# Performance work log

Hardware: AMD Instinct MI355X
Metric: run time of the kernel (lower is better)

## Reference

```python
import jax, jax.numpy as jnp
import numpy as np

B, S, HID, NH = 4, 2048, 128, 8
D_MODEL = HID * NH  # per-Q/K/V dim = 1024


def setup_inputs() -> dict:
    key = jax.random.key(0)
    k1, k2, k3, k4, k5 = jax.random.split(key, 5)
    return {
        "x": jax.random.normal(k1, (B, S, HID), dtype=jnp.float32),
        "W_qkv": jax.random.normal(k2, (HID, 3 * D_MODEL), dtype=jnp.float32) * 0.02,
        "b_qkv": jax.random.normal(k3, (3 * D_MODEL,), dtype=jnp.float32) * 0.02,
        "W_o": jax.random.normal(k4, (D_MODEL, HID), dtype=jnp.float32) * 0.02,
        "b_o": jax.random.normal(k5, (HID,), dtype=jnp.float32) * 0.02,
        "num_heads": NH,
    }


def reference(x, W_qkv, b_qkv, W_o, b_o, num_heads):
    b, s, _ = x.shape
    qkv = x @ W_qkv + b_qkv                      # [b, s, 3*d_model]
    Q, K, V = jnp.split(qkv, 3, axis=2)          # each [b, s, d_model]
    d_full = Q.shape[-1]                         # n_heads*headsize (faithful to source)
    hs = d_full // num_heads
    # [b, s, h*hs] -> [b, h, s, hs]
    def to_heads(t):
        return t.reshape(b, s, num_heads, hs).transpose(0, 2, 1, 3)
    Qh, Kh, Vh = to_heads(Q), to_heads(K), to_heads(V)
    scores = jnp.einsum('bhsc,bhtc->bhst', Qh, Kh)
    # multiplicative upper-triangular mask (faithful quirk of source)
    tri = jnp.triu(jnp.ones((s, s), dtype=scores.dtype))
    A_pre = scores * tri / jnp.sqrt(jnp.asarray(d_full, dtype=scores.dtype))
    # softmax over dim=1 == heads axis (faithful quirk of source)
    A = jax.nn.softmax(A_pre, axis=1)
    out = jnp.einsum('bhst,bhtc->bhsc', A, Vh)   # [b, h, s, hs]
    out = out.transpose(0, 2, 1, 3).reshape(b, s, d_full)
    return out @ W_o + b_o                        # [b, s, hidden]
```

## Files before the change

kernel.cpp:

```cpp
#include <hip/hip_runtime.h>
#include <hip/hip_bf16.h>

#define SEQ 2048
#define NHEAD 8
#define HDIM 128

typedef __attribute__((ext_vector_type(8))) short bf16x8;
typedef __attribute__((ext_vector_type(4))) float f32x4;
typedef long i64;
typedef unsigned long long u64;

static __device__ __forceinline__ short f2b(float f) {
  union { float f; unsigned u; } v; v.f = f;
  unsigned r = (v.u + 0x7FFFu + ((v.u >> 16) & 1u)) >> 16;
  return (short)(unsigned short)r;
}
static __device__ __forceinline__ float b2f(short b) {
  union { unsigned u; float f; } v; v.u = ((unsigned)(unsigned short)b) << 16;
  return v.f;
}
static __device__ __forceinline__ unsigned f2e4m3(float x) {
  union { float f; unsigned u; } v; v.f = x;
  unsigned s = (v.u >> 24) & 0x80u;
  unsigned a = v.u & 0x7FFFFFFFu;
  if (a > 0x43E00000u) a = 0x43E00000u;
  if (a < 0x3C800000u) {
    union { unsigned u; float f; } w; w.u = a;
    return s | (unsigned)(int)(w.f * 512.0f + 0.5f);
  }
  a += 0x7FFFFu + ((a >> 20) & 1u);
  return s | (((a >> 23) - 120u) << 3) | ((a >> 20) & 7u);
}

#if defined(__has_builtin)
#if __has_builtin(__builtin_amdgcn_cvt_pk_fp8_f32)
#define HAVE_HW_FP8 1
#endif
#endif
static __device__ __forceinline__ unsigned cvt_pk_fp8(float a, float b) {
#ifdef HAVE_HW_FP8
  return (unsigned)__builtin_amdgcn_cvt_pk_fp8_f32(a, b, 0, false) & 0xFFFFu;
#else
  return f2e4m3(a) | (f2e4m3(b) << 8);
#endif
}
static __device__ __forceinline__ unsigned cvt_fp8_1(float a) {
  return cvt_pk_fp8(a, 0.0f) & 0xFFu;
}

#define BARRIER_RAW() asm volatile("s_waitcnt lgkmcnt(0)\n\ts_barrier" ::: "memory")

__global__ __launch_bounds__(256) void k_cvt_x(const float* __restrict__ x,
                                               short* __restrict__ xb) {
  int i = blockIdx.x * blockDim.x + threadIdx.x;
  const float4* p = reinterpret_cast<const float4*>(x) + (size_t)i * 2;
  float4 a = p[0], c = p[1];
  bf16x8 o;
  o[0] = f2b(a.x); o[1] = f2b(a.y); o[2] = f2b(a.z); o[3] = f2b(a.w);
  o[4] = f2b(c.x); o[5] = f2b(c.y); o[6] = f2b(c.z); o[7] = f2b(c.w);
  reinterpret_cast<bf16x8*>(xb)[i] = o;
}

__global__ __launch_bounds__(256) void k_wqkv(const float* __restrict__ w,
                                              short* __restrict__ wt) {
  int tid = blockIdx.x * blockDim.x + threadIdx.x;
  int k = tid & 127, j = tid >> 7;
  wt[tid] = f2b(w[(size_t)k * 3072 + j]);
}

__global__ __launch_bounds__(256) void k_wo(const float* __restrict__ w,
                                            short* __restrict__ wt) {
  int tid = blockIdx.x * blockDim.x + threadIdx.x;
  int k = tid & 1023, c = tid >> 10;
  wt[tid] = f2b(w[(size_t)k * 128 + c]);
}

__global__ __launch_bounds__(256) void k_qkv(const short* __restrict__ xb,
                                             const short* __restrict__ wqt,
                                             const float* __restrict__ bias,
                                             unsigned char* __restrict__ Qf,
                                             unsigned char* __restrict__ Kf,
                                             unsigned char* __restrict__ Vt) {
  int wave = threadIdx.x >> 6, lane = threadIdx.x & 63;
  int lr = lane & 15, lg = lane >> 4;
  int m0 = blockIdx.y * 64 + wave * 16;
  int j0 = blockIdx.x * 128;

  bf16x8 a[4];
#pragma unroll
  for (int ks = 0; ks < 4; ++ks)
    a[ks] = *reinterpret_cast<const bf16x8*>(xb + (size_t)(m0 + lr) * 128 + ks * 32 + lg * 8);

  f32x4 acc[8];
#pragma unroll
  for (int nf = 0; nf < 8; ++nf) acc[nf] = (f32x4){0.f, 0.f, 0.f, 0.f};

#pragma unroll
  for (int ks = 0; ks < 4; ++ks) {
#pragma unroll
    for (int nf = 0; nf < 8; ++nf) {
      bf16x8 bfr = *reinterpret_cast<const bf16x8*>(
          wqt + (size_t)(j0 + nf * 16 + lr) * 128 + ks * 32 + lg * 8);
      acc[nf] = __builtin_amdgcn_mfma_f32_16x16x32_bf16(a[ks], bfr, acc[nf], 0, 0, 0);
    }
  }

  int bb = m0 >> 11;
  int sbase = m0 & 2047;
#pragma unroll
  for (int nf = 0; nf < 8; ++nf) {
    int j = j0 + nf * 16 + lr;
    float bv = bias[j];
    int sel = j >> 10;
    int jj = j & 1023;
    int h = jj >> 7, c = jj & 127;
    size_t bh = (size_t)(bb * NHEAD + h);
    if (sel == 2) {
      unsigned lo = cvt_pk_fp8((acc[nf][0] + bv) * 16.0f, (acc[nf][1] + bv) * 16.0f);
      unsigned hi = cvt_pk_fp8((acc[nf][2] + bv) * 16.0f, (acc[nf][3] + bv) * 16.0f);
      *reinterpret_cast<unsigned*>(Vt + (bh * HDIM + c) * SEQ + sbase + lg * 4) =
          lo | (hi << 16);
    } else {
      unsigned char* dst = (sel ? Kf : Qf);
#pragma unroll
      for (int r = 0; r < 4; ++r) {
        int s = sbase + lg * 4 + r;
        dst[(bh * SEQ + s) * HDIM + c] = (unsigned char)cvt_fp8_1((acc[nf][r] + bv) * 4.0f);
      }
    }
  }
}

__global__ __launch_bounds__(256) void k_tot(const unsigned char* __restrict__ Vt,
                                             float* __restrict__ Tot8) {
  __shared__ float lut[256];
  {
    int t = threadIdx.x;
    unsigned e = (t >> 3) & 15u, m = t & 7u;
    float mag = e ? ldexpf((float)(8 + m), (int)e - 10) : ldexpf((float)m, -9);
    lut[t] = (t & 128) ? -mag : mag;
  }
  __syncthreads();
  int wave = threadIdx.x >> 6, lane = threadIdx.x & 63;
  int row = blockIdx.x * 4 + wave;
  const unsigned char* p = Vt + (size_t)row * SEQ;
  float s = 0.f;
#pragma unroll
  for (int k = 0; k < 4; ++k) {
    u64 v = *reinterpret_cast<const u64*>(p + k * 512 + lane * 8);
#pragma unroll
    for (int j = 0; j < 8; ++j) s += lut[(unsigned)(v >> (8 * j)) & 255u];
  }
#pragma unroll
  for (int off = 32; off > 0; off >>= 1) s += __shfl_down(s, off, 64);
  if (lane == 0) Tot8[row] = s * 0.0078125f;
}

__global__ __launch_bounds__(512, 4) void k_attn(const unsigned char* __restrict__ Qf,
                                                 const unsigned char* __restrict__ Kf,
                                                 const unsigned char* __restrict__ Vt,
                                                 short* __restrict__ Part) {
  __shared__ float Sm[8][32][36];
  __shared__ unsigned char Pm[8][32][40];

  int tid = threadIdx.x;
  int h = (__builtin_amdgcn_readfirstlane(tid) >> 6) & 7;
  int lane = tid & 63, lr = lane & 15, lg = lane >> 4;
  int bid = blockIdx.x;
  int xcd = bid & 7, slot = bid >> 3;
  int b = xcd >> 1, tc = xcd & 1;
  int c0 = (slot < 32) ? slot : (95 - slot);
  int rb = c0 * 32;

  const unsigned char* Qh = Qf + ((size_t)(b * NHEAD + h)) * SEQ * HDIM;
  const unsigned char* Kh = Kf + ((size_t)(b * NHEAD + h)) * SEQ * HDIM;
  const unsigned char* Vh = Vt + ((size_t)(b * NHEAD + h)) * HDIM * SEQ;
  short* PartT = Part + (size_t)tc * (size_t)(4 * SEQ) * 1024;

  int sl = tid >> 4;
  int t2 = (tid & 15) * 2;
  const float SC = 0.001953125f;

  i64 qa[2][4];
#pragma unroll
  for (int rf = 0; rf < 2; ++rf)
#pragma unroll
    for (int ks = 0; ks < 4; ++ks)
      qa[rf][ks] = *reinterpret_cast<const i64*>(
          Qh + (size_t)(rb + rf * 16 + lr) * HDIM + ks * 32 + lg * 8);

  f32x4 oa[2][8];
#pragma unroll
  for (int rf = 0; rf < 2; ++rf)
#pragma unroll
    for (int cf = 0; cf < 8; ++cf) oa[rf][cf] = (f32x4){0.f, 0.f, 0.f, 0.f};

  int ttF = 62 + tc;

#pragma unroll 1
  for (int tt = ttF; tt >= c0; tt -= 2) {
    int t0 = tt * 32;
    i64 vf[8];
#pragma unroll
    for (int cf = 0; cf < 8; ++cf)
      vf[cf] = *reinterpret_cast<const i64*>(Vh + (size_t)(cf * 16 + lr) * SEQ + t0 + lg * 8);
    i64 kf[2][4];
#pragma unroll
    for (int nf = 0; nf < 2; ++nf)
#pragma unroll
      for (int ks = 0; ks < 4; ++ks)
        kf[nf][ks] = *reinterpret_cast<const i64*>(
            Kh + (size_t)(t0 + nf * 16 + lr) * HDIM + ks * 32 + lg * 8);

    __builtin_amdgcn_s_setprio(1);
#pragma unroll
    for (int rf = 0; rf < 2; ++rf) {
      f32x4 s0v = (f32x4){0.f, 0.f, 0.f, 0.f}, s1v = (f32x4){0.f, 0.f, 0.f, 0.f};
#pragma unroll
      for (int ks = 0; ks < 4; ++ks) {
        s0v = __builtin_amdgcn_mfma_f32_16x16x32_fp8_fp8(qa[rf][ks], kf[0][ks], s0v, 0, 0, 0);
        s1v = __builtin_amdgcn_mfma_f32_16x16x32_fp8_fp8(qa[rf][ks], kf[1][ks], s1v, 0, 0, 0);
      }
      int rowb = rf * 16 + lg * 4;
#pragma unroll
      for (int r = 0; r < 4; ++r) {
        Sm[h][rowb + r][lr] = s0v[r];
        Sm[h][rowb + r][16 + lr] = s1v[r];
      }
    }
    __builtin_amdgcn_s_setprio(0);
    BARRIER_RAW();

    {
      int sg = rb + sl;
      int tg = t0 + t2;
      float e[8][2];
      float sm0 = 0.f, sm1 = 0.f;
#pragma unroll
      for (int hh = 0; hh < 8; ++hh) {
        float2 v = *reinterpret_cast<const float2*>(&Sm[hh][sl][t2]);
        e[hh][0] = __expf(v.x * SC); sm0 += e[hh][0];
        e[hh][1] = __expf(v.y * SC); sm1 += e[hh][1];
      }
      float inv0 = 8.0f / sm0, inv1 = 8.0f / sm1;
      bool mk0 = (tg >= sg), mk1 = (tg + 1 >= sg);
#pragma unroll
      for (int hh = 0; hh < 8; ++hh) {
        float a0 = mk0 ? (e[hh][0] * inv0 - 1.0f) : 0.0f;
        float a1 = mk1 ? (e[hh][1] * inv1 - 1.0f) : 0.0f;
        *reinterpret_cast<unsigned short*>(&Pm[hh][sl][t2]) =
            (unsigned short)cvt_pk_fp8(a0, a1);
      }
    }
    BARRIER_RAW();

    __builtin_amdgcn_s_setprio(1);
#pragma unroll
    for (int rf = 0; rf < 2; ++rf) {
      i64 pa = *reinterpret_cast<const i64*>(&Pm[h][rf * 16 + lr][lg * 8]);
#pragma unroll
      for (int cf = 0; cf < 8; ++cf)
        oa[rf][cf] = __builtin_amdgcn_mfma_f32_16x16x32_fp8_fp8(pa, vf[cf], oa[rf][cf], 0, 0, 0);
    }
    __builtin_amdgcn_s_setprio(0);
  }

  short* baseP = PartT + (size_t)(b * SEQ + rb) * 1024 + h * HDIM;
#pragma unroll
  for (int rf = 0; rf < 2; ++rf)
#pragma unroll
    for (int cf = 0; cf < 8; ++cf)
#pragma unroll
      for (int r = 0; r < 4; ++r)
        baseP[(size_t)(rf * 16 + lg * 4 + r) * 1024 + cf * 16 + lr] =
            f2b(oa[rf][cf][r] * 0.0078125f);
}

__global__ __launch_bounds__(256) void k_out(const short* __restrict__ Part,
                                             const float* __restrict__ Tot8,
                                             const short* __restrict__ wot,
                                             const float* __restrict__ bo,
                                             float* __restrict__ out) {
  const size_t PSZ = (size_t)(4 * SEQ) * 1024;
  int wave = threadIdx.x >> 6, lane = threadIdx.x & 63;
  int lr = lane & 15, lg = lane >> 4;
  int m0 = blockIdx.x * 32 + (wave & 1) * 16;
  int n0 = (wave >> 1) * 64;
  int bb = m0 >> 11;
  const float* t8 = Tot8 + ((size_t)bb << 10);

  f32x4 acc[4];
#pragma unroll
  for (int nf = 0; nf < 4; ++nf) acc[nf] = (f32x4){0.f, 0.f, 0.f, 0.f};

  for (int ks = 0; ks < 32; ++ks) {
    int kb = ks * 32 + lg * 8;
    const short* pr = Part + (size_t)(m0 + lr) * 1024 + kb;
    bf16x8 q0 = *reinterpret_cast<const bf16x8*>(pr);
    bf16x8 q1 = *reinterpret_cast<const bf16x8*>(pr + PSZ);
    float4 ta = *reinterpret_cast<const float4*>(t8 + kb);
    float4 tb = *reinterpret_cast<const float4*>(t8 + kb + 4);
    float tv[8] = {ta.x, ta.y, ta.z, ta.w, tb.x, tb.y, tb.z, tb.w};
    bf16x8 af;
#pragma unroll
    for (int j = 0; j < 8; ++j)
      af[j] = f2b(b2f(q0[j]) + b2f(q1[j]) + tv[j]);
#pragma unroll
    for (int nf = 0; nf < 4; ++nf) {
      bf16x8 bfr = *reinterpret_cast<const bf16x8*>(
          wot + (size_t)(n0 + nf * 16 + lr) * 1024 + kb);
      acc[nf] = __builtin_amdgcn_mfma_f32_16x16x32_bf16(af, bfr, acc[nf], 0, 0, 0);
    }
  }
#pragma unroll
  for (int nf = 0; nf < 4; ++nf) {
    int c = n0 + nf * 16 + lr;
    float bv = bo[c];
#pragma unroll
    for (int r = 0; r < 4; ++r)
      out[(size_t)(m0 + lg * 4 + r) * 128 + c] = acc[nf][r] + bv;
  }
}

extern "C" void kernel_launch(void* const* d_in, const int* in_sizes, int n_in,
                              void* d_out, int out_size, void* d_ws, size_t ws_size,
                              hipStream_t stream) {
  const float* x    = (const float*)d_in[0];
  const float* wqkv = (const float*)d_in[1];
  const float* bqkv = (const float*)d_in[2];
  const float* wo   = (const float*)d_in[3];
  const float* bo   = (const float*)d_in[4];

  char* ws = (char*)d_ws;
  const size_t MB = (size_t)1 << 20;
  short* xb          = (short*)(ws + 0);
  short* wqt         = (short*)(ws + 2 * MB);
  short* wot         = (short*)(ws + 3 * MB);
  unsigned char* Qf  = (unsigned char*)(ws + 4 * MB);
  unsigned char* Kf  = (unsigned char*)(ws + 12 * MB);
  unsigned char* Vt  = (unsigned char*)(ws + 20 * MB);
  float* Tot8        = (float*)(ws + 28 * MB);
  short* Part        = (short*)(ws + 29 * MB);

  hipLaunchKernelGGL(k_cvt_x, dim3(512), dim3(256), 0, stream, x, xb);
  hipLaunchKernelGGL(k_wqkv, dim3(1536), dim3(256), 0, stream, wqkv, wqt);
  hipLaunchKernelGGL(k_wo, dim3(512), dim3(256), 0, stream, wo, wqt == nullptr ? wot : wot);
  hipLaunchKernelGGL(k_qkv, dim3(24, 128), dim3(256), 0, stream, xb, wqt, bqkv, Qf, Kf, Vt);
  hipLaunchKernelGGL(k_tot, dim3(1024), dim3(256), 0, stream, Vt, Tot8);
  hipLaunchKernelGGL(k_attn, dim3(512), dim3(512), 0, stream, Qf, Kf, Vt, Part);
  hipLaunchKernelGGL(k_out, dim3(256), dim3(256), 0, stream, Part, Tot8, wot, bo, (float*)d_out);
}
```

Baseline: 277.3 us.

## Use 64-row query tiles with four-way key split and fp8 partial outputs

```diff
diff --git a/kernel.cpp b/kernel.cpp
--- a/kernel.cpp
+++ b/kernel.cpp
@@ -156,131 +156,151 @@
   if (lane == 0) Tot8[row] = s * 0.0078125f;
 }
 
-__global__ __launch_bounds__(512, 4) void k_attn(const unsigned char* __restrict__ Qf,
+__global__ __launch_bounds__(512, 2) void k_attn(const unsigned char* __restrict__ Qf,
                                                  const unsigned char* __restrict__ Kf,
                                                  const unsigned char* __restrict__ Vt,
-                                                 short* __restrict__ Part) {
-  __shared__ float Sm[8][32][36];
-  __shared__ unsigned char Pm[8][32][40];
-
+                                                 unsigned char* __restrict__ Part) {
+  __shared__ float Sm[8][64][36];
+  __shared__ unsigned char Pm[8][64][40];
+
+  const size_t PSZ = (size_t)(4 * SEQ) * 1024;
   int tid = threadIdx.x;
   int h = (__builtin_amdgcn_readfirstlane(tid) >> 6) & 7;
   int lane = tid & 63, lr = lane & 15, lg = lane >> 4;
   int bid = blockIdx.x;
   int xcd = bid & 7, slot = bid >> 3;
-  int b = xcd >> 1, tc = xcd & 1;
-  int c0 = (slot < 32) ? slot : (95 - slot);
-  int rb = c0 * 32;
+  int b = xcd >> 1, tcA = xcd & 1;
+  int p = slot >> 1, tcB = slot & 1;
+  int tc = tcB * 2 + tcA;
 
   const unsigned char* Qh = Qf + ((size_t)(b * NHEAD + h)) * SEQ * HDIM;
   const unsigned char* Kh = Kf + ((size_t)(b * NHEAD + h)) * SEQ * HDIM;
   const unsigned char* Vh = Vt + ((size_t)(b * NHEAD + h)) * HDIM * SEQ;
-  short* PartT = Part + (size_t)tc * (size_t)(4 * SEQ) * 1024;
-
-  int sl = tid >> 4;
-  int t2 = (tid & 15) * 2;
+  unsigned char* PartT = Part + (size_t)tc * PSZ;
+
+  int sl = tid >> 3;
+  int t4 = (tid & 7) * 4;
   const float SC = 0.001953125f;
 
-  i64 qa[2][4];
-#pragma unroll
-  for (int rf = 0; rf < 2; ++rf)
-#pragma unroll
-    for (int ks = 0; ks < 4; ++ks)
-      qa[rf][ks] = *reinterpret_cast<const i64*>(
-          Qh + (size_t)(rb + rf * 16 + lr) * HDIM + ks * 32 + lg * 8);
-
-  f32x4 oa[2][8];
-#pragma unroll
-  for (int rf = 0; rf < 2; ++rf)
-#pragma unroll
-    for (int cf = 0; cf < 8; ++cf) oa[rf][cf] = (f32x4){0.f, 0.f, 0.f, 0.f};
-
-  int ttF = 62 + tc;
-
 #pragma unroll 1
-  for (int tt = ttF; tt >= c0; tt -= 2) {
-    int t0 = tt * 32;
-    i64 vf[8];
-#pragma unroll
-    for (int cf = 0; cf < 8; ++cf)
-      vf[cf] = *reinterpret_cast<const i64*>(Vh + (size_t)(cf * 16 + lr) * SEQ + t0 + lg * 8);
-    i64 kf[2][4];
-#pragma unroll
-    for (int nf = 0; nf < 2; ++nf)
+  for (int ph = 0; ph < 2; ++ph) {
+    int c0 = ph ? (31 - p) : p;
+    int rb = c0 * 64;
+
+    i64 qa[4][4];
+#pragma unroll
+    for (int rf = 0; rf < 4; ++rf)
 #pragma unroll
       for (int ks = 0; ks < 4; ++ks)
-        kf[nf][ks] = *reinterpret_cast<const i64*>(
-            Kh + (size_t)(t0 + nf * 16 + lr) * HDIM + ks * 32 + lg * 8);
-
-    __builtin_amdgcn_s_setprio(1);
-#pragma unroll
-    for (int rf = 0; rf < 2; ++rf) {
-      f32x4 s0v = (f32x4){0.f, 0.f, 0.f, 0.f}, s1v = (f32x4){0.f, 0.f, 0.f, 0.f};
-#pragma unroll
-      for (int ks = 0; ks < 4; ++ks) {
-        s0v = __builtin_amdgcn_mfma_f32_16x16x32_fp8_fp8(qa[rf][ks], kf[0][ks], s0v, 0, 0, 0);
-        s1v = __builtin_amdgcn_mfma_f32_16x16x32_fp8_fp8(qa[rf][ks], kf[1][ks], s1v, 0, 0, 0);
+        qa[rf][ks] = *reinterpret_cast<const i64*>(
+            Qh + (size_t)(rb + rf * 16 + lr) * HDIM + ks * 32 + lg * 8);
+
+    f32x4 oa[4][8];
+#pragma unroll
+    for (int rf = 0; rf < 4; ++rf)
+#pragma unroll
+      for (int cf = 0; cf < 8; ++cf) oa[rf][cf] = (f32x4){0.f, 0.f, 0.f, 0.f};
+
+    int ttF = 60 + tc, ttMin = 2 * c0;
+
+#pragma unroll 1
+    for (int tt = ttF; tt >= ttMin; tt -= 4) {
+      int t0 = tt * 32;
+      i64 vf[8];
+#pragma unroll
+      for (int cf = 0; cf < 8; ++cf)
+        vf[cf] = *reinterpret_cast<const i64*>(Vh + (size_t)(cf * 16 + lr) * SEQ + t0 + lg * 8);
+      i64 kf[2][4];
+#pragma unroll
+      for (int nf = 0; nf < 2; ++nf)
+#pragma unroll
+        for (int ks = 0; ks < 4; ++ks)
+          kf[nf][ks] = *reinterpret_cast<const i64*>(
+              Kh + (size_t)(t0 + nf * 16 + lr) * HDIM + ks * 32 + lg * 8);
+
+      __builtin_amdgcn_s_setprio(1);
+#pragma unroll
+      for (int rf = 0; rf < 4; ++rf) {
+        f32x4 s0v = (f32x4){0.f, 0.f, 0.f, 0.f}, s1v = (f32x4){0.f, 0.f, 0.f, 0.f};
+#pragma unroll
+        for (int ks = 0; ks < 4; ++ks) {
+          s0v = __builtin_amdgcn_mfma_f32_16x16x32_fp8_fp8(qa[rf][ks], kf[0][ks], s0v, 0, 0, 0);
+          s1v = __builtin_amdgcn_mfma_f32_16x16x32_fp8_fp8(qa[rf][ks], kf[1][ks], s1v, 0, 0, 0);
+        }
+        int rowb = rf * 16 + lg * 4;
+#pragma unroll
+        for (int r = 0; r < 4; ++r) {
+          Sm[h][rowb + r][lr] = s0v[r];
+          Sm[h][rowb + r][16 + lr] = s1v[r];
+        }
       }
-      int rowb = rf * 16 + lg * 4;
-#pragma unroll
-      for (int r = 0; r < 4; ++r) {
-        Sm[h][rowb + r][lr] = s0v[r];
-        Sm[h][rowb + r][16 + lr] = s1v[r];
+      __builtin_amdgcn_s_setprio(0);
+      BARRIER_RAW();
+
+      {
+        int sg = rb + sl;
+#pragma unroll 1
+        for (int bt = 0; bt < 2; ++bt) {
+          int tcb = t4 + 2 * bt;
+          int tg = t0 + tcb;
+          float e[8][2];
+          float sm0 = 0.f, sm1 = 0.f;
+#pragma unroll
+          for (int hh = 0; hh < 8; ++hh) {
+            float2 v = *reinterpret_cast<const float2*>(&Sm[hh][sl][tcb]);
+            e[hh][0] = __expf(v.x * SC); sm0 += e[hh][0];
+            e[hh][1] = __expf(v.y * SC); sm1 += e[hh][1];
+          }
+          float inv0 = 8.0f / sm0, inv1 = 8.0f / sm1;
+          bool mk0 = (tg >= sg), mk1 = (tg + 1 >= sg);
+#pragma unroll
+          for (int hh = 0; hh < 8; ++hh) {
+            float a0 = mk0 ? (e[hh][0] * inv0 - 1.0f) : 0.0f;
+            float a1 = mk1 ? (e[hh][1] * inv1 - 1.0f) : 0.0f;
+            *reinterpret_cast<unsigned short*>(&Pm[hh][sl][tcb]) =
+                (unsigned short)cvt_pk_fp8(a0, a1);
+          }
+        }
       }
-    }
-    __builtin_amdgcn_s_setprio(0);
-    BARRIER_RAW();
-
-    {
-      int sg = rb + sl;
-      int tg = t0 + t2;
-      float e[8][2];
-      float sm0 = 0.f, sm1 = 0.f;
-#pragma unroll
-      for (int hh = 0; hh < 8; ++hh) {
-        float2 v = *reinterpret_cast<const float2*>(&Sm[hh][sl][t2]);
-        e[hh][0] = __expf(v.x * SC); sm0 += e[hh][0];
-        e[hh][1] = __expf(v.y * SC); sm1 += e[hh][1];
+      BARRIER_RAW();
+
+      __builtin_amdgcn_s_setprio(1);
+#pragma unroll
+      for (int rf = 0; rf < 4; ++rf) {
+        i64 pa = *reinterpret_cast<const i64*>(&Pm[h][rf * 16 + lr][lg * 8]);
+#pragma unroll
+        for (int cf = 0; cf < 8; ++cf)
+          oa[rf][cf] = __builtin_amdgcn_mfma_f32_16x16x32_fp8_fp8(pa, vf[cf], oa[rf][cf], 0, 0, 0);
       }
-      float inv0 = 8.0f / sm0, inv1 = 8.0f / sm1;
-      bool mk0 = (tg >= sg), mk1 = (tg + 1 >= sg);
-#pragma unroll
-      for (int hh = 0; hh < 8; ++hh) {
-        float a0 = mk0 ? (e[hh][0] * inv0 - 1.0f) : 0.0f;
-        float a1 = mk1 ? (e[hh][1] * inv1 - 1.0f) : 0.0f;
-        *reinterpret_cast<unsigned short*>(&Pm[hh][sl][t2]) =
-            (unsigned short)cvt_pk_fp8(a0, a1);
-      }
-    }
-    BARRIER_RAW();
-
-    __builtin_amdgcn_s_setprio(1);
-#pragma unroll
-    for (int rf = 0; rf < 2; ++rf) {
-      i64 pa = *reinterpret_cast<const i64*>(&Pm[h][rf * 16 + lr][lg * 8]);
+      __builtin_amdgcn_s_setprio(0);
+    }
+
+    unsigned char* baseP = PartT + (size_t)(b * SEQ + rb) * 1024 + h * HDIM;
+#pragma unroll
+    for (int rf = 0; rf < 4; ++rf)
 #pragma unroll
       for (int cf = 0; cf < 8; ++cf)
-        oa[rf][cf] = __builtin_amdgcn_mfma_f32_16x16x32_fp8_fp8(pa, vf[cf], oa[rf][cf], 0, 0, 0);
-    }
-    __builtin_amdgcn_s_setprio(0);
-  }
-
-  short* baseP = PartT + (size_t)(b * SEQ + rb) * 1024 + h * HDIM;
-#pragma unroll
-  for (int rf = 0; rf < 2; ++rf)
-#pragma unroll
-    for (int cf = 0; cf < 8; ++cf)
-#pragma unroll
-      for (int r = 0; r < 4; ++r)
-        baseP[(size_t)(rf * 16 + lg * 4 + r) * 1024 + cf * 16 + lr] =
-            f2b(oa[rf][cf][r] * 0.0078125f);
-}
-
-__global__ __launch_bounds__(256) void k_out(const short* __restrict__ Part,
+#pragma unroll
+        for (int r = 0; r < 4; ++r)
+          baseP[(size_t)(rf * 16 + lg * 4 + r) * 1024 + cf * 16 + lr] =
+              (unsigned char)cvt_fp8_1(oa[rf][cf][r] * 0.0078125f);
+  }
+}
+
+__global__ __launch_bounds__(256) void k_out(const unsigned char* __restrict__ Part,
                                              const float* __restrict__ Tot8,
                                              const short* __restrict__ wot,
                                              const float* __restrict__ bo,
                                              float* __restrict__ out) {
+  __shared__ float lut[256];
+  {
+    int t = threadIdx.x;
+    unsigned e = (t >> 3) & 15u, m = t & 7u;
+    float mag = e ? ldexpf((float)(8 + m), (int)e - 10) : ldexpf((float)m, -9);
+    lut[t] = (t & 128) ? -mag : mag;
+  }
+  __syncthreads();
+
   const size_t PSZ = (size_t)(4 * SEQ) * 1024;
   int wave = threadIdx.x >> 6, lane = threadIdx.x & 63;
   int lr = lane & 15, lg = lane >> 4;
@@ -295,16 +315,23 @@
 
   for (int ks = 0; ks < 32; ++ks) {
     int kb = ks * 32 + lg * 8;
-    const short* pr = Part + (size_t)(m0 + lr) * 1024 + kb;
-    bf16x8 q0 = *reinterpret_cast<const bf16x8*>(pr);
-    bf16x8 q1 = *reinterpret_cast<const bf16x8*>(pr + PSZ);
+    const unsigned char* pr = Part + (size_t)(m0 + lr) * 1024 + kb;
+    u64 q0 = *reinterpret_cast<const u64*>(pr);
+    u64 q1 = *reinterpret_cast<const u64*>(pr + PSZ);
+    u64 q2 = *reinterpret_cast<const u64*>(pr + 2 * PSZ);
+    u64 q3 = *reinterpret_cast<const u64*>(pr + 3 * PSZ);
     float4 ta = *reinterpret_cast<const float4*>(t8 + kb);
     float4 tb = *reinterpret_cast<const float4*>(t8 + kb + 4);
     float tv[8] = {ta.x, ta.y, ta.z, ta.w, tb.x, tb.y, tb.z, tb.w};
     bf16x8 af;
 #pragma unroll
-    for (int j = 0; j < 8; ++j)
-      af[j] = f2b(b2f(q0[j]) + b2f(q1[j]) + tv[j]);
+    for (int j = 0; j < 8; ++j) {
+      float f = lut[(unsigned)(q0 >> (8 * j)) & 255u] +
+                lut[(unsigned)(q1 >> (8 * j)) & 255u] +
+                lut[(unsigned)(q2 >> (8 * j)) & 255u] +
+                lut[(unsigned)(q3 >> (8 * j)) & 255u] + tv[j];
+      af[j] = f2b(f);
+    }
 #pragma unroll
     for (int nf = 0; nf < 4; ++nf) {
       bf16x8 bfr = *reinterpret_cast<const bf16x8*>(
@@ -340,13 +367,13 @@
   unsigned char* Kf  = (unsigned char*)(ws + 12 * MB);
   unsigned char* Vt  = (unsigned char*)(ws + 20 * MB);
   float* Tot8        = (float*)(ws + 28 * MB);
-  short* Part        = (short*)(ws + 29 * MB);
+  unsigned char* Part = (unsigned char*)(ws + 29 * MB);
 
   hipLaunchKernelGGL(k_cvt_x, dim3(512), dim3(256), 0, stream, x, xb);
   hipLaunchKernelGGL(k_wqkv, dim3(1536), dim3(256), 0, stream, wqkv, wqt);
-  hipLaunchKernelGGL(k_wo, dim3(512), dim3(256), 0, stream, wo, wqt == nullptr ? wot : wot);
+  hipLaunchKernelGGL(k_wo, dim3(512), dim3(256), 0, stream, wo, wot);
   hipLaunchKernelGGL(k_qkv, dim3(24, 128), dim3(256), 0, stream, xb, wqt, bqkv, Qf, Kf, Vt);
   hipLaunchKernelGGL(k_tot, dim3(1024), dim3(256), 0, stream, Vt, Tot8);
-  hipLaunchKernelGGL(k_attn, dim3(512), dim3(512), 0, stream, Qf, Kf, Vt, Part);
+  hipLaunchKernelGGL(k_attn, dim3(256), dim3(512), 0, stream, Qf, Kf, Vt, Part);
   hipLaunchKernelGGL(k_out, dim3(256), dim3(256), 0, stream, Part, Tot8, wot, bo, (float*)d_out);
 }
```

After: 270.6 us. -2.4%, faster.

## Fold output projection into V before attention and reduce heads in-register

Applied to the files above, without the earlier changes.

```diff
diff --git a/kernel.cpp b/kernel.cpp
--- a/kernel.cpp
+++ b/kernel.cpp
@@ -2,11 +2,14 @@
 #include <hip/hip_bf16.h>
 
 #define SEQ 2048
+#define NBATCH 4
 #define NHEAD 8
 #define HDIM 128
 
 typedef __attribute__((ext_vector_type(8))) short bf16x8;
 typedef __attribute__((ext_vector_type(4))) float f32x4;
+typedef __attribute__((ext_vector_type(4))) _Float16 f16x4;
+typedef __attribute__((ext_vector_type(2))) __fp16 h16x2;
 typedef long i64;
 typedef unsigned long long u64;
 
@@ -47,8 +50,11 @@
 static __device__ __forceinline__ unsigned cvt_fp8_1(float a) {
   return cvt_pk_fp8(a, 0.0f) & 0xFFu;
 }
-
-#define BARRIER_RAW() asm volatile("s_waitcnt lgkmcnt(0)\n\ts_barrier" ::: "memory")
+static __device__ __forceinline__ f16x4 pack4h(h16x2 lo, h16x2 hi) {
+  union { h16x2 a[2]; f16x4 b; } u;
+  u.a[0] = lo; u.a[1] = hi;
+  return u.b;
+}
 
 __global__ __launch_bounds__(256) void k_cvt_x(const float* __restrict__ x,
                                                short* __restrict__ xb) {
@@ -80,7 +86,7 @@
                                              const float* __restrict__ bias,
                                              unsigned char* __restrict__ Qf,
                                              unsigned char* __restrict__ Kf,
-                                             unsigned char* __restrict__ Vt) {
+                                             short* __restrict__ Vb) {
   int wave = threadIdx.x >> 6, lane = threadIdx.x & 63;
   int lr = lane & 15, lg = lane >> 4;
   int m0 = blockIdx.y * 64 + wave * 16;
@@ -116,10 +122,11 @@
     int h = jj >> 7, c = jj & 127;
     size_t bh = (size_t)(bb * NHEAD + h);
     if (sel == 2) {
-      unsigned lo = cvt_pk_fp8((acc[nf][0] + bv) * 16.0f, (acc[nf][1] + bv) * 16.0f);
-      unsigned hi = cvt_pk_fp8((acc[nf][2] + bv) * 16.0f, (acc[nf][3] + bv) * 16.0f);
-      *reinterpret_cast<unsigned*>(Vt + (bh * HDIM + c) * SEQ + sbase + lg * 4) =
-          lo | (hi << 16);
+#pragma unroll
+      for (int r = 0; r < 4; ++r) {
+        int s = sbase + lg * 4 + r;
+        Vb[(bh * SEQ + s) * HDIM + c] = f2b(acc[nf][r] + bv);
+      }
     } else {
       unsigned char* dst = (sel ? Kf : Qf);
 #pragma unroll
@@ -131,8 +138,171 @@
   }
 }
 
-__global__ __launch_bounds__(256) void k_tot(const unsigned char* __restrict__ Vt,
-                                             float* __restrict__ Tot8) {
+__global__ __launch_bounds__(256) void k_vw(const short* __restrict__ wot,
+                                            const short* __restrict__ Vb,
+                                            _Float16* __restrict__ VWf) {
+  int w = threadIdx.x >> 6, lane = threadIdx.x & 63, lr = lane & 15, lg = lane >> 4;
+  int bh = blockIdx.y, h = bh & 7;
+  int tile = blockIdx.x * 4 + w;
+  int t0 = tile * 16;
+
+  f32x4 acc[8];
+#pragma unroll
+  for (int cf = 0; cf < 8; ++cf) acc[cf] = (f32x4){0.f, 0.f, 0.f, 0.f};
+
+#pragma unroll
+  for (int ks = 0; ks < 4; ++ks) {
+    bf16x8 bfr = *reinterpret_cast<const bf16x8*>(
+        Vb + ((size_t)bh * SEQ + t0 + lr) * HDIM + ks * 32 + lg * 8);
+#pragma unroll
+    for (int cf = 0; cf < 8; ++cf) {
+      bf16x8 af = *reinterpret_cast<const bf16x8*>(
+          wot + (size_t)(cf * 16 + lr) * 1024 + h * 128 + ks * 32 + lg * 8);
+      acc[cf] = __builtin_amdgcn_mfma_f32_16x16x32_bf16(af, bfr, acc[cf], 0, 0, 0);
+    }
+  }
+  _Float16* dst = VWf + ((size_t)bh * 128 + tile) * 128 * 16;
+#pragma unroll
+  for (int cf = 0; cf < 8; ++cf)
+#pragma unroll
+    for (int r = 0; r < 4; ++r)
+      dst[(size_t)(cf * 16 + 4 * lg + r) * 16 + lr] = (_Float16)acc[cf][r];
+}
+
+__global__ __launch_bounds__(256) void k_tot(const short* __restrict__ Vb,
+                                             float* __restrict__ Totv) {
+  __shared__ float sh[16][128];
+  int bh = blockIdx.x;
+  int i = threadIdx.x & 15, g = threadIdx.x >> 4;
+  const short* p = Vb + (size_t)bh * SEQ * HDIM + i * 8;
+  float s[8] = {0, 0, 0, 0, 0, 0, 0, 0};
+  for (int r = g; r < SEQ; r += 16) {
+    bf16x8 v = *reinterpret_cast<const bf16x8*>(p + (size_t)r * HDIM);
+#pragma unroll
+    for (int j = 0; j < 8; ++j) s[j] += b2f(v[j]);
+  }
+#pragma unroll
+  for (int j = 0; j < 8; ++j) sh[g][i * 8 + j] = s[j];
+  __syncthreads();
+  if (threadIdx.x < 128) {
+    float t = 0;
+#pragma unroll
+    for (int g2 = 0; g2 < 16; ++g2) t += sh[g2][threadIdx.x];
+    Totv[bh * 128 + threadIdx.x] = t;
+  }
+}
+
+__global__ __launch_bounds__(256) void k_totw(const float* __restrict__ Totv,
+                                              const float* __restrict__ wo,
+                                              float* __restrict__ Totw) {
+  __shared__ float sh[128];
+  int b = blockIdx.x, c = threadIdx.x & 127, h2 = threadIdx.x >> 7;
+  float s = 0.f;
+  for (int j = h2 * 512; j < h2 * 512 + 512; ++j)
+    s += Totv[b * 1024 + j] * wo[(size_t)j * 128 + c];
+  if (h2) sh[c] = s;
+  __syncthreads();
+  if (!h2) Totw[b * 128 + c] = 0.125f * (s + sh[c]);
+}
+
+__global__ __launch_bounds__(256, 2) void k_attn(const unsigned char* __restrict__ Qf,
+                                                 const unsigned char* __restrict__ Kf,
+                                                 const _Float16* __restrict__ VWf,
+                                                 unsigned char* __restrict__ Part) {
+  int tid = threadIdx.x;
+  int w = tid >> 6, lane = tid & 63, lr = lane & 15, lg = lane >> 4;
+  int bid = blockIdx.x;
+  int xcd = bid & 7, slot = bid >> 3;
+  int b = xcd >> 1, tcA = xcd & 1;
+  int tcB = slot & 3, q = slot >> 2;
+  int tc = (tcB << 1) | tcA;
+  const float SC = 0.001953125f;
+  const size_t BH = (size_t)SEQ * HDIM;
+
+#pragma unroll 1
+  for (int ph = 0; ph < 2; ++ph) {
+    int st = ph ? (127 - (q * 4 + w)) : (q * 4 + w);
+    int rb = st * 16;
+
+    i64 qa[8][4];
+#pragma unroll
+    for (int h = 0; h < 8; ++h)
+#pragma unroll
+      for (int ks = 0; ks < 4; ++ks)
+        qa[h][ks] = *reinterpret_cast<const i64*>(
+            Qf + (size_t)(b * 8 + h) * BH + (size_t)(rb + lr) * HDIM + ks * 32 + lg * 8);
+
+    f32x4 oa[8];
+#pragma unroll
+    for (int cf = 0; cf < 8; ++cf) oa[cf] = (f32x4){0.f, 0.f, 0.f, 0.f};
+
+    int ttF = 120 + tc;
+#pragma unroll 1
+    for (int tt = ttF; tt >= st; tt -= 8) {
+      int t0 = tt * 16;
+      f32x4 S[8];
+#pragma unroll
+      for (int h = 0; h < 8; ++h) {
+        const unsigned char* Kh = Kf + (size_t)(b * 8 + h) * BH + (size_t)(t0 + lr) * HDIM;
+        f32x4 s = (f32x4){0.f, 0.f, 0.f, 0.f};
+#pragma unroll
+        for (int ks = 0; ks < 4; ++ks) {
+          i64 kfr = *reinterpret_cast<const i64*>(Kh + ks * 32 + lg * 8);
+          s = __builtin_amdgcn_mfma_f32_16x16x32_fp8_fp8(kfr, qa[h][ks], s, 0, 0, 0);
+        }
+        S[h] = s;
+      }
+      f16x4 P[8];
+      {
+        float ex[8][4];
+        float sm0 = 0.f, sm1 = 0.f, sm2 = 0.f, sm3 = 0.f;
+#pragma unroll
+        for (int h = 0; h < 8; ++h) {
+          ex[h][0] = __expf(S[h][0] * SC); sm0 += ex[h][0];
+          ex[h][1] = __expf(S[h][1] * SC); sm1 += ex[h][1];
+          ex[h][2] = __expf(S[h][2] * SC); sm2 += ex[h][2];
+          ex[h][3] = __expf(S[h][3] * SC); sm3 += ex[h][3];
+        }
+        int sg = rb + lr;
+        int tb = t0 + 4 * lg;
+        float i0 = 8.0f / sm0, i1 = 8.0f / sm1, i2 = 8.0f / sm2, i3 = 8.0f / sm3;
+        bool m0 = (tb >= sg), m1 = (tb + 1 >= sg), m2 = (tb + 2 >= sg), m3 = (tb + 3 >= sg);
+#pragma unroll
+        for (int h = 0; h < 8; ++h) {
+          float p0 = m0 ? ex[h][0] * i0 - 1.0f : 0.0f;
+          float p1 = m1 ? ex[h][1] * i1 - 1.0f : 0.0f;
+          float p2 = m2 ? ex[h][2] * i2 - 1.0f : 0.0f;
+          float p3 = m3 ? ex[h][3] * i3 - 1.0f : 0.0f;
+          P[h] = pack4h(__builtin_amdgcn_cvt_pkrtz(p0, p1),
+                        __builtin_amdgcn_cvt_pkrtz(p2, p3));
+        }
+      }
+#pragma unroll
+      for (int h = 0; h < 8; ++h) {
+        const _Float16* VWh = VWf + ((size_t)(b * 8 + h) * 128 + tt) * (128 * 16);
+#pragma unroll
+        for (int cf = 0; cf < 8; ++cf) {
+          f16x4 vw = *reinterpret_cast<const f16x4*>(VWh + (size_t)(cf * 16 + lr) * 16 + 4 * lg);
+          oa[cf] = __builtin_amdgcn_mfma_f32_16x16x16f16(vw, P[h], oa[cf], 0, 0, 0);
+        }
+      }
+    }
+
+    unsigned char* Pt = Part + (size_t)tc * ((size_t)4 * SEQ * 128) +
+                        ((size_t)(b * SEQ + rb + lr)) * 128;
+#pragma unroll
+    for (int cf = 0; cf < 8; ++cf) {
+      unsigned u = cvt_pk_fp8(oa[cf][0] * 4.0f, oa[cf][1] * 4.0f) |
+                   (cvt_pk_fp8(oa[cf][2] * 4.0f, oa[cf][3] * 4.0f) << 16);
+      *reinterpret_cast<unsigned*>(Pt + cf * 16 + lg * 4) = u;
+    }
+  }
+}
+
+__global__ __launch_bounds__(256) void k_fin(const unsigned char* __restrict__ Part,
+                                             const float* __restrict__ Totw,
+                                             const float* __restrict__ bo,
+                                             float* __restrict__ out) {
   __shared__ float lut[256];
   {
     int t = threadIdx.x;
@@ -141,185 +311,14 @@
     lut[t] = (t & 128) ? -mag : mag;
   }
   __syncthreads();
-  int wave = threadIdx.x >> 6, lane = threadIdx.x & 63;
-  int row = blockIdx.x * 4 + wave;
-  const unsigned char* p = Vt + (size_t)row * SEQ;
+  const size_t PSZ = (size_t)4 * SEQ * 128;
+  int idx = blockIdx.x * 256 + threadIdx.x;
+  int c = idx & 127, sg = idx >> 7;
+  int b = sg >> 11;
   float s = 0.f;
 #pragma unroll
-  for (int k = 0; k < 4; ++k) {
-    u64 v = *reinterpret_cast<const u64*>(p + k * 512 + lane * 8);
-#pragma unroll
-    for (int j = 0; j < 8; ++j) s += lut[(unsigned)(v >> (8 * j)) & 255u];
-  }
-#pragma unroll
-  for (int off = 32; off > 0; off >>= 1) s += __shfl_down(s, off, 64);
-  if (lane == 0) Tot8[row] = s * 0.0078125f;
-}
-
-__global__ __launch_bounds__(512, 4) void k_attn(const unsigned char* __restrict__ Qf,
-                                                 const unsigned char* __restrict__ Kf,
-                                                 const unsigned char* __restrict__ Vt,
-                                                 short* __restrict__ Part) {
-  __shared__ float Sm[8][32][36];
-  __shared__ unsigned char Pm[8][32][40];
-
-  int tid = threadIdx.x;
-  int h = (__builtin_amdgcn_readfirstlane(tid) >> 6) & 7;
-  int lane = tid & 63, lr = lane & 15, lg = lane >> 4;
-  int bid = blockIdx.x;
-  int xcd = bid & 7, slot = bid >> 3;
-  int b = xcd >> 1, tc = xcd & 1;
-  int c0 = (slot < 32) ? slot : (95 - slot);
-  int rb = c0 * 32;
-
-  const unsigned char* Qh = Qf + ((size_t)(b * NHEAD + h)) * SEQ * HDIM;
-  const unsigned char* Kh = Kf + ((size_t)(b * NHEAD + h)) * SEQ * HDIM;
-  const unsigned char* Vh = Vt + ((size_t)(b * NHEAD + h)) * HDIM * SEQ;
-  short* PartT = Part + (size_t)tc * (size_t)(4 * SEQ) * 1024;
-
-  int sl = tid >> 4;
-  int t2 = (tid & 15) * 2;
-  const float SC = 0.001953125f;
-
-  i64 qa[2][4];
-#pragma unroll
-  for (int rf = 0; rf < 2; ++rf)
-#pragma unroll
-    for (int ks = 0; ks < 4; ++ks)
-      qa[rf][ks] = *reinterpret_cast<const i64*>(
-          Qh + (size_t)(rb + rf * 16 + lr) * HDIM + ks * 32 + lg * 8);
-
-  f32x4 oa[2][8];
-#pragma unroll
-  for (int rf = 0; rf < 2; ++rf)
-#pragma unroll
-    for (int cf = 0; cf < 8; ++cf) oa[rf][cf] = (f32x4){0.f, 0.f, 0.f, 0.f};
-
-  int ttF = 62 + tc;
-
-#pragma unroll 1
-  for (int tt = ttF; tt >= c0; tt -= 2) {
-    int t0 = tt * 32;
-    i64 vf[8];
-#pragma unroll
-    for (int cf = 0; cf < 8; ++cf)
-      vf[cf] = *reinterpret_cast<const i64*>(Vh + (size_t)(cf * 16 + lr) * SEQ + t0 + lg * 8);
-    i64 kf[2][4];
-#pragma unroll
-    for (int nf = 0; nf < 2; ++nf)
-#pragma unroll
-      for (int ks = 0; ks < 4; ++ks)
-        kf[nf][ks] = *reinterpret_cast<const i64*>(
-            Kh + (size_t)(t0 + nf * 16 + lr) * HDIM + ks * 32 + lg * 8);
-
-    __builtin_amdgcn_s_setprio(1);
-#pragma unroll
-    for (int rf = 0; rf < 2; ++rf) {
-      f32x4 s0v = (f32x4){0.f, 0.f, 0.f, 0.f}, s1v = (f32x4){0.f, 0.f, 0.f, 0.f};
-#pragma unroll
-      for (int ks = 0; ks < 4; ++ks) {
-        s0v = __builtin_amdgcn_mfma_f32_16x16x32_fp8_fp8(qa[rf][ks], kf[0][ks], s0v, 0, 0, 0);
-        s1v = __builtin_amdgcn_mfma_f32_16x16x32_fp8_fp8(qa[rf][ks], kf[1][ks], s1v, 0, 0, 0);
-      }
-      int rowb = rf * 16 + lg * 4;
-#pragma unroll
-      for (int r = 0; r < 4; ++r) {
-        Sm[h][rowb + r][lr] = s0v[r];
-        Sm[h][rowb + r][16 + lr] = s1v[r];
-      }
-    }
-    __builtin_amdgcn_s_setprio(0);
-    BARRIER_RAW();
-
-    {
-      int sg = rb + sl;
-      int tg = t0 + t2;
-      float e[8][2];
-      float sm0 = 0.f, sm1 = 0.f;
-#pragma unroll
-      for (int hh = 0; hh < 8; ++hh) {
-        float2 v = *reinterpret_cast<const float2*>(&Sm[hh][sl][t2]);
-        e[hh][0] = __expf(v.x * SC); sm0 += e[hh][0];
-        e[hh][1] = __expf(v.y * SC); sm1 += e[hh][1];
-      }
-      float inv0 = 8.0f / sm0, inv1 = 8.0f / sm1;
-      bool mk0 = (tg >= sg), mk1 = (tg + 1 >= sg);
-#pragma unroll
-      for (int hh = 0; hh < 8; ++hh) {
-        float a0 = mk0 ? (e[hh][0] * inv0 - 1.0f) : 0.0f;
-        float a1 = mk1 ? (e[hh][1] * inv1 - 1.0f) : 0.0f;
-        *reinterpret_cast<unsigned short*>(&Pm[hh][sl][t2]) =
-            (unsigned short)cvt_pk_fp8(a0, a1);
-      }
-    }
-    BARRIER_RAW();
-
-    __builtin_amdgcn_s_setprio(1);
-#pragma unroll
-    for (int rf = 0; rf < 2; ++rf) {
-      i64 pa = *reinterpret_cast<const i64*>(&Pm[h][rf * 16 + lr][lg * 8]);
-#pragma unroll
-      for (int cf = 0; cf < 8; ++cf)
-        oa[rf][cf] = __builtin_amdgcn_mfma_f32_16x16x32_fp8_fp8(pa, vf[cf], oa[rf][cf], 0, 0, 0);
-    }
-    __builtin_amdgcn_s_setprio(0);
-  }
-
-  short* baseP = PartT + (size_t)(b * SEQ + rb) * 1024 + h * HDIM;
-#pragma unroll
-  for (int rf = 0; rf < 2; ++rf)
-#pragma unroll
-    for (int cf = 0; cf < 8; ++cf)
-#pragma unroll
-      for (int r = 0; r < 4; ++r)
-        baseP[(size_t)(rf * 16 + lg * 4 + r) * 1024 + cf * 16 + lr] =
-            f2b(oa[rf][cf][r] * 0.0078125f);
-}
-
-__global__ __launch_bounds__(256) void k_out(const short* __restrict__ Part,
-                                             const float* __restrict__ Tot8,
-                                             const short* __restrict__ wot,
-                                             const float* __restrict__ bo,
-                                             float* __restrict__ out) {
-  const size_t PSZ = (size_t)(4 * SEQ) * 1024;
-  int wave = threadIdx.x >> 6, lane = threadIdx.x & 63;
-  int lr = lane & 15, lg = lane >> 4;
-  int m0 = blockIdx.x * 32 + (wave & 1) * 16;
-  int n0 = (wave >> 1) * 64;
-  int bb = m0 >> 11;
-  const float* t8 = Tot8 + ((size_t)bb << 10);
-
-  f32x4 acc[4];
-#pragma unroll
-  for (int nf = 0; nf < 4; ++nf) acc[nf] = (f32x4){0.f, 0.f, 0.f, 0.f};
-
-  for (int ks = 0; ks < 32; ++ks) {
-    int kb = ks * 32 + lg * 8;
-    const short* pr = Part + (size_t)(m0 + lr) * 1024 + kb;
-    bf16x8 q0 = *reinterpret_cast<const bf16x8*>(pr);
-    bf16x8 q1 = *reinterpret_cast<const bf16x8*>(pr + PSZ);
-    float4 ta = *reinterpret_cast<const float4*>(t8 + kb);
-    float4 tb = *reinterpret_cast<const float4*>(t8 + kb + 4);
-    float tv[8] = {ta.x, ta.y, ta.z, ta.w, tb.x, tb.y, tb.z, tb.w};
-    bf16x8 af;
-#pragma unroll
-    for (int j = 0; j < 8; ++j)
-      af[j] = f2b(b2f(q0[j]) + b2f(q1[j]) + tv[j]);
-#pragma unroll
-    for (int nf = 0; nf < 4; ++nf) {
-      bf16x8 bfr = *reinterpret_cast<const bf16x8*>(
-          wot + (size_t)(n0 + nf * 16 + lr) * 1024 + kb);
-      acc[nf] = __builtin_amdgcn_mfma_f32_16x16x32_bf16(af, bfr, acc[nf], 0, 0, 0);
-    }
-  }
-#pragma unroll
-  for (int nf = 0; nf < 4; ++nf) {
-    int c = n0 + nf * 16 + lr;
-    float bv = bo[c];
-#pragma unroll
-    for (int r = 0; r < 4; ++r)
-      out[(size_t)(m0 + lg * 4 + r) * 128 + c] = acc[nf][r] + bv;
-  }
+  for (int t = 0; t < 8; ++t) s += lut[Part[(size_t)t * PSZ + (size_t)sg * 128 + c]];
+  out[(size_t)sg * 128 + c] = s * 0.03125f + Totw[b * 128 + c] + bo[c];
 }
 
 extern "C" void kernel_launch(void* const* d_in, const int* in_sizes, int n_in,
@@ -333,20 +332,24 @@
 
   char* ws = (char*)d_ws;
   const size_t MB = (size_t)1 << 20;
-  short* xb          = (short*)(ws + 0);
-  short* wqt         = (short*)(ws + 2 * MB);
-  short* wot         = (short*)(ws + 3 * MB);
-  unsigned char* Qf  = (unsigned char*)(ws + 4 * MB);
-  unsigned char* Kf  = (unsigned char*)(ws + 12 * MB);
-  unsigned char* Vt  = (unsigned char*)(ws + 20 * MB);
-  float* Tot8        = (float*)(ws + 28 * MB);
-  short* Part        = (short*)(ws + 29 * MB);
+  short* xb           = (short*)(ws + 0);
+  short* wqt          = (short*)(ws + 2 * MB);
+  short* wot          = (short*)(ws + 3 * MB);
+  unsigned char* Qf   = (unsigned char*)(ws + 4 * MB);
+  unsigned char* Kf   = (unsigned char*)(ws + 12 * MB);
+  short* Vb           = (short*)(ws + 20 * MB);
+  _Float16* VWf       = (_Float16*)(ws + 36 * MB);
+  float* Totv         = (float*)(ws + 52 * MB);
+  float* Totw         = (float*)(ws + 53 * MB);
+  unsigned char* Part = (unsigned char*)(ws + 54 * MB);
 
   hipLaunchKernelGGL(k_cvt_x, dim3(512), dim3(256), 0, stream, x, xb);
   hipLaunchKernelGGL(k_wqkv, dim3(1536), dim3(256), 0, stream, wqkv, wqt);
-  hipLaunchKernelGGL(k_wo, dim3(512), dim3(256), 0, stream, wo, wqt == nullptr ? wot : wot);
-  hipLaunchKernelGGL(k_qkv, dim3(24, 128), dim3(256), 0, stream, xb, wqt, bqkv, Qf, Kf, Vt);
-  hipLaunchKernelGGL(k_tot, dim3(1024), dim3(256), 0, stream, Vt, Tot8);
-  hipLaunchKernelGGL(k_attn, dim3(512), dim3(512), 0, stream, Qf, Kf, Vt, Part);
-  hipLaunchKernelGGL(k_out, dim3(256), dim3(256), 0, stream, Part, Tot8, wot, bo, (float*)d_out);
-}
+  hipLaunchKernelGGL(k_wo, dim3(512), dim3(256), 0, stream, wo, wot);
+  hipLaunchKernelGGL(k_qkv, dim3(24, 128), dim3(256), 0, stream, xb, wqt, bqkv, Qf, Kf, Vb);
+  hipLaunchKernelGGL(k_vw, dim3(32, 32), dim3(256), 0, stream, wot, Vb, VWf);
+  hipLaunchKernelGGL(k_tot, dim3(32), dim3(256), 0, stream, Vb, Totv);
+  hipLaunchKernelGGL(k_totw, dim3(4), dim3(256), 0, stream, Totv, wo, Totw);
+  hipLaunchKernelGGL(k_attn, dim3(512), dim3(256), 0, stream, Qf, Kf, VWf, Part);
+  hipLaunchKernelGGL(k_fin, dim3(4096), dim3(256), 0, stream, Part, Totw, bo, (float*)d_out);
+}
```

Measured after the change: 586.5 us. 2.12x slower.
